# Kernel optimization log

Measured on AMD Instinct MI355X. Metric: run time of the kernel, lower is better.

## Reference

```python
import jax, jax.numpy as jnp
import numpy as np

N_NODES = 100000
N_EDGES = 3200000
NUM_FEATURES = 128
HIDDEN = 16


def _gcn_norm(edge_index, num_nodes):
    # Add self-loops and compute symmetric normalization D^{-1/2} (A+I) D^{-1/2}
    loops = jnp.arange(num_nodes, dtype=edge_index.dtype)
    row = jnp.concatenate([edge_index[0], loops])  # source j
    col = jnp.concatenate([edge_index[1], loops])  # target i
    ones = jnp.ones(row.shape[0], dtype=jnp.float32)
    deg = jax.ops.segment_sum(ones, col, num_segments=num_nodes)
    deg_inv_sqrt = jnp.where(deg > 0, jax.lax.rsqrt(deg), 0.0)
    norm = deg_inv_sqrt[row] * deg_inv_sqrt[col]  # [E + N]
    return row, col, norm


def _gcn_conv(x, row, col, norm, W, b, num_nodes):
    h = x @ W                                   # [N, out] linear first (PyG order)
    msg = h[row] * norm[:, None]                # gather + edge-wise scale
    out = jax.ops.segment_sum(msg, col, num_segments=num_nodes)  # scatter-add
    return out + b                              # bias after aggregation (PyG)


def setup_inputs() -> dict:
    key = jax.random.key(0)
    k1, k2, k3, k4, k5 = jax.random.split(key, 5)
    x = jax.random.normal(k1, (N_NODES, NUM_FEATURES), dtype=jnp.float32)
    edge_index = jax.random.randint(k2, (2, N_EDGES), 0, N_NODES, dtype=jnp.int64)
    # Glorot-style init for GCNConv linear weights
    W1 = jax.random.normal(k3, (NUM_FEATURES, HIDDEN), dtype=jnp.float32) / np.sqrt(NUM_FEATURES)
    b1 = jnp.zeros((HIDDEN,), dtype=jnp.float32)
    W2 = jax.random.normal(k4, (HIDDEN, 1), dtype=jnp.float32) / np.sqrt(HIDDEN)
    b2 = jnp.zeros((1,), dtype=jnp.float32)
    return {"x": x, "edge_index": edge_index, "W1": W1, "b1": b1, "W2": W2, "b2": b2}


def reference(x, edge_index, W1, b1, W2, b2):
    num_nodes = x.shape[0]
    row, col, norm = _gcn_norm(edge_index, num_nodes)  # shared by both layers
    h = _gcn_conv(x, row, col, norm, W1, b1, num_nodes)
    h = jax.nn.relu(h)
    out = _gcn_conv(h, row, col, norm, W2, b2, num_nodes)
    return out
```

## Files before the change

### kernel.cpp

```cpp
#include <hip/hip_runtime.h>
#include <hip/hip_fp16.h>


#define CB 8
#define CAP 9216
#define TILE 4096

__global__ void k_init_gcur(int* __restrict__ gcur, int nb) {
    int b = blockIdx.x * blockDim.x + threadIdx.x;
    if (b < nb) gcur[b] = b * CAP;
}

__global__ void __launch_bounds__(512) k_partition(
        const int* __restrict__ row, const int* __restrict__ col,
        int* __restrict__ gcur, int* __restrict__ ebuf, int e, int nb) {
    __shared__ int hist[512];
    __shared__ int lbase[512];
    __shared__ int gdelta[512];
    __shared__ int sval[TILE];
    __shared__ unsigned short sbkt[TILE];
    const int base = blockIdx.x * TILE;
    const int cnt = min(TILE, e - base);
    const int t = threadIdx.x;
    hist[t] = 0;
    __syncthreads();
#pragma unroll
    for (int k = 0; k < TILE / 512; ++k) {
        int i = base + (k << 9) + t;
        if (i < e) atomicAdd(&hist[col[i] >> CB], 1);
    }
    __syncthreads();
    int v = hist[t];
    lbase[t] = v;
    __syncthreads();
    for (int off = 1; off < 512; off <<= 1) {
        int add = (t >= off) ? lbase[t - off] : 0;
        __syncthreads();
        lbase[t] += add;
        __syncthreads();
    }
    int excl = lbase[t] - v;
    __syncthreads();
    lbase[t] = excl;
    int gb = v ? atomicAdd(&gcur[t], v) : 0;
    gdelta[t] = gb - excl;
    hist[t] = excl;
    __syncthreads();
#pragma unroll
    for (int k = 0; k < TILE / 512; ++k) {
        int i = base + (k << 9) + t;
        if (i < e) {
            int c = col[i], r = row[i];
            int b = c >> CB;
            int p = atomicAdd(&hist[b], 1);
            sval[p] = ((c & ((1 << CB) - 1)) << 17) | r;
            sbkt[p] = (unsigned short)b;
        }
    }
    __syncthreads();
    for (int j = t; j < cnt; j += 512) {
        int b = sbkt[j];
        int p = gdelta[b] + j;
        if (p < (b + 1) * CAP) ebuf[p] = sval[j];
    }
}

__global__ void __launch_bounds__(256) k_bucket(
        const int* __restrict__ ebuf, const int* __restrict__ gcur,
        int* __restrict__ begA, int* __restrict__ endA, int* __restrict__ ssrc,
        float* __restrict__ dis, int n) {
    __shared__ int hist[256];
    __shared__ int sc[256];
    const int b = blockIdx.x, t = threadIdx.x;
    const int base = b * CAP;
    const int cnt = min(gcur[b] - base, CAP);
    hist[t] = 0;
    __syncthreads();
    for (int j = t; j < cnt; j += 256) atomicAdd(&hist[ebuf[base + j] >> 17], 1);
    __syncthreads();
    int v = hist[t];
    sc[t] = v;
    __syncthreads();
    for (int off = 1; off < 256; off <<= 1) {
        int add = (t >= off) ? sc[t - off] : 0;
        __syncthreads();
        sc[t] += add;
        __syncthreads();
    }
    int excl = sc[t] - v;
    int node = (b << CB) + t;
    if (node < n) {
        begA[node] = base + excl;
        endA[node] = base + excl + v;
        dis[node] = rsqrtf((float)(v + 1));
    }
    hist[t] = excl;
    __syncthreads();
    for (int j = t; j < cnt; j += 256) {
        int val = ebuf[base + j];
        int p = atomicAdd(&hist[val >> 17], 1);
        ssrc[base + p] = val & 0x1FFFF;
    }
}

__global__ void k_gemm1(const float* __restrict__ x, const float* __restrict__ W1,
                        const float* __restrict__ dis, __half* __restrict__ gh, int n) {
    __shared__ float wt[16 * 128];
    for (int t = threadIdx.x; t < 2048; t += blockDim.x) {
        int j = t >> 7, k = t & 127;
        wt[t] = W1[k * 16 + j];
    }
    __syncthreads();
    int r = blockIdx.x * blockDim.x + threadIdx.x;
    if (r >= n) return;
    const float4* x4 = (const float4*)(x + (size_t)r * 128);
    const float4* w4 = (const float4*)wt;
    float acc[16];
#pragma unroll
    for (int j = 0; j < 16; ++j) acc[j] = 0.f;
    for (int k4 = 0; k4 < 32; ++k4) {
        float4 vv = x4[k4];
#pragma unroll
        for (int j = 0; j < 16; ++j) {
            float4 w = w4[j * 32 + k4];
            acc[j] += vv.x * w.x + vv.y * w.y + vv.z * w.z + vv.w * w.w;
        }
    }
    float d = dis[r];
    __half2 hh[8];
#pragma unroll
    for (int j = 0; j < 8; ++j)
        hh[j] = __floats2half2_rn(d * acc[2 * j], d * acc[2 * j + 1]);
    uint4* o = (uint4*)(gh + (size_t)r * 16);
    const uint4* src = (const uint4*)hh;
    o[0] = src[0];
    o[1] = src[1];
}

__global__ void k_gather1(const int* __restrict__ begA, const int* __restrict__ endA,
                          const int* __restrict__ ssrc,
                          const __half2* __restrict__ g2, const float* __restrict__ dis,
                          const float* __restrict__ b1, const float* __restrict__ W2,
                          float* __restrict__ tbuf, int n) {
    int t = blockIdx.x * blockDim.x + threadIdx.x;
    if (t >= n * 8) return;
    int i = t >> 3, f2 = t & 7;
    float di = dis[i];
    int beg = begA[i], end = endA[i];
    float2 acc = __half22float2(g2[(size_t)i * 8 + f2]);
    for (int e = beg; e < end; ++e) {
        float2 v = __half22float2(g2[(size_t)ssrc[e] * 8 + f2]);
        acc.x += v.x;
        acc.y += v.y;
    }
    int f = f2 * 2;
    float u = fmaxf(di * acc.x + b1[f], 0.f) * W2[f]
            + fmaxf(di * acc.y + b1[f + 1], 0.f) * W2[f + 1];
#pragma unroll
    for (int m = 4; m >= 1; m >>= 1) u += __shfl_xor(u, m, 8);
    if (f2 == 0) tbuf[i] = di * u;
}

__global__ void k_gather2(const int* __restrict__ begA, const int* __restrict__ endA,
                          const int* __restrict__ ssrc,
                          const float* __restrict__ tbuf, const float* __restrict__ dis,
                          const float* __restrict__ b2, float* __restrict__ out, int n) {
    int t = blockIdx.x * blockDim.x + threadIdx.x;
    if (t >= n * 8) return;
    int i = t >> 3, l = t & 7;
    int beg = begA[i], end = endA[i];
    float acc = (l == 0) ? tbuf[i] : 0.f;
    for (int e = beg + l; e < end; e += 8) acc += tbuf[ssrc[e]];
#pragma unroll
    for (int m = 4; m >= 1; m >>= 1) acc += __shfl_xor(acc, m, 8);
    if (l == 0) out[i] = dis[i] * acc + b2[0];
}

extern "C" void kernel_launch(void* const* d_in, const int* in_sizes, int n_in,
                              void* d_out, int out_size, void* d_ws, size_t ws_size,
                              hipStream_t stream) {
    const float* x  = (const float*)d_in[0];
    const int*   ei = (const int*)d_in[1];
    const float* W1 = (const float*)d_in[2];
    const float* b1 = (const float*)d_in[3];
    const float* W2 = (const float*)d_in[4];
    const float* b2 = (const float*)d_in[5];
    float* out = (float*)d_out;

    const int N = in_sizes[0] / 128;
    const int E = in_sizes[1] / 2;
    const int* row = ei;
    const int* col = ei + E;
    const int NB = (N + 255) >> CB;
    const size_t PADE = (size_t)NB * CAP;

    size_t bigsz = PADE > (size_t)N * 8 ? PADE : (size_t)N * 8;
    int*    ebuf = (int*)d_ws;
    __half* gh   = (__half*)d_ws;
    int*    ssrc = (int*)d_ws + bigsz;
    float*  dis  = (float*)(ssrc + PADE);
    float*  tbuf = dis + N;
    int*    begA = (int*)(tbuf + N);
    int*    endA = begA + N;
    int*    gcur = endA + N;

    auto cdiv = [](int a, int b) { return (a + b - 1) / b; };

    k_init_gcur<<<cdiv(NB, 256),    256, 0, stream>>>(gcur, NB);
    k_partition<<<cdiv(E, TILE),    512, 0, stream>>>(row, col, gcur, ebuf, E, NB);
    k_bucket   <<<NB,               256, 0, stream>>>(ebuf, gcur, begA, endA, ssrc, dis, N);
    k_gemm1    <<<cdiv(N, 256),     256, 0, stream>>>(x, W1, dis, gh, N);
    k_gather1  <<<cdiv(N * 8, 256), 256, 0, stream>>>(begA, endA, ssrc, (const __half2*)gh,
                                                      dis, b1, W2, tbuf, N);
    k_gather2  <<<cdiv(N * 8, 256), 256, 0, stream>>>(begA, endA, ssrc, tbuf, dis, b2, out, N);
}
```

Baseline: 238.9 us.

## Replace per-node CSR build with bucket-level LDS atomic aggregation

Drops the second counting-sort pass inside each 256-node bucket, along with the begA/endA/ssrc arrays. The k_bucket kernel shrinks to a degree-only kernel. Both aggregation layers now run one 1024-thread block per bucket: each block streams the bucket's unsorted edges, gathers the source features with one-step prefetch, and accumulates into shared memory with float atomics before applying the epilogue. This removes the per-node segment walk and the scatter of sorted indices. In exchange it relies on heavy LDS float atomics, 16 per edge in layer 1, which may contend, and it makes the summation order nondeterministic.

```diff
diff --git a/kernel.cpp b/kernel.cpp
--- a/kernel.cpp
+++ b/kernel.cpp
@@ -65,12 +65,10 @@
     }
 }
 
-__global__ void __launch_bounds__(256) k_bucket(
+__global__ void __launch_bounds__(256) k_deg(
         const int* __restrict__ ebuf, const int* __restrict__ gcur,
-        int* __restrict__ begA, int* __restrict__ endA, int* __restrict__ ssrc,
         float* __restrict__ dis, int n) {
     __shared__ int hist[256];
-    __shared__ int sc[256];
     const int b = blockIdx.x, t = threadIdx.x;
     const int base = b * CAP;
     const int cnt = min(gcur[b] - base, CAP);
@@ -78,29 +76,8 @@
     __syncthreads();
     for (int j = t; j < cnt; j += 256) atomicAdd(&hist[ebuf[base + j] >> 17], 1);
     __syncthreads();
-    int v = hist[t];
-    sc[t] = v;
-    __syncthreads();
-    for (int off = 1; off < 256; off <<= 1) {
-        int add = (t >= off) ? sc[t - off] : 0;
-        __syncthreads();
-        sc[t] += add;
-        __syncthreads();
-    }
-    int excl = sc[t] - v;
     int node = (b << CB) + t;
-    if (node < n) {
-        begA[node] = base + excl;
-        endA[node] = base + excl + v;
-        dis[node] = rsqrtf((float)(v + 1));
-    }
-    hist[t] = excl;
-    __syncthreads();
-    for (int j = t; j < cnt; j += 256) {
-        int val = ebuf[base + j];
-        int p = atomicAdd(&hist[val >> 17], 1);
-        ssrc[base + p] = val & 0x1FFFF;
-    }
+    if (node < n) dis[node] = rsqrtf((float)(hist[t] + 1));
 }
 
 __global__ void k_gemm1(const float* __restrict__ x, const float* __restrict__ W1,
@@ -137,43 +114,102 @@
     o[1] = src[1];
 }
 
-__global__ void k_gather1(const int* __restrict__ begA, const int* __restrict__ endA,
-                          const int* __restrict__ ssrc,
-                          const __half2* __restrict__ g2, const float* __restrict__ dis,
-                          const float* __restrict__ b1, const float* __restrict__ W2,
-                          float* __restrict__ tbuf, int n) {
-    int t = blockIdx.x * blockDim.x + threadIdx.x;
-    if (t >= n * 8) return;
-    int i = t >> 3, f2 = t & 7;
-    float di = dis[i];
-    int beg = begA[i], end = endA[i];
-    float2 acc = __half22float2(g2[(size_t)i * 8 + f2]);
-    for (int e = beg; e < end; ++e) {
-        float2 v = __half22float2(g2[(size_t)ssrc[e] * 8 + f2]);
-        acc.x += v.x;
-        acc.y += v.y;
-    }
-    int f = f2 * 2;
-    float u = fmaxf(di * acc.x + b1[f], 0.f) * W2[f]
-            + fmaxf(di * acc.y + b1[f + 1], 0.f) * W2[f + 1];
-#pragma unroll
-    for (int m = 4; m >= 1; m >>= 1) u += __shfl_xor(u, m, 8);
-    if (f2 == 0) tbuf[i] = di * u;
-}
-
-__global__ void k_gather2(const int* __restrict__ begA, const int* __restrict__ endA,
-                          const int* __restrict__ ssrc,
-                          const float* __restrict__ tbuf, const float* __restrict__ dis,
-                          const float* __restrict__ b2, float* __restrict__ out, int n) {
-    int t = blockIdx.x * blockDim.x + threadIdx.x;
-    if (t >= n * 8) return;
-    int i = t >> 3, l = t & 7;
-    int beg = begA[i], end = endA[i];
-    float acc = (l == 0) ? tbuf[i] : 0.f;
-    for (int e = beg + l; e < end; e += 8) acc += tbuf[ssrc[e]];
-#pragma unroll
-    for (int m = 4; m >= 1; m >>= 1) acc += __shfl_xor(acc, m, 8);
-    if (l == 0) out[i] = dis[i] * acc + b2[0];
+__device__ inline void unpack8(uint4 u, float* f) {
+    const __half2* h = (const __half2*)&u;
+#pragma unroll
+    for (int k = 0; k < 4; ++k) {
+        float2 t2 = __half22float2(h[k]);
+        f[2 * k] = t2.x;
+        f[2 * k + 1] = t2.y;
+    }
+}
+
+__global__ void __launch_bounds__(1024) k_fused1(
+        const int* __restrict__ ebuf, const int* __restrict__ gcur,
+        const uint4* __restrict__ gq, const float* __restrict__ dis,
+        const float* __restrict__ b1, const float* __restrict__ W2,
+        float* __restrict__ tbuf, int n) {
+    __shared__ float agg[256 * 17];
+    __shared__ float sB[16], sW[16];
+    const int b = blockIdx.x, t = threadIdx.x;
+    const int base = b * CAP;
+    const int cnt = min(gcur[b] - base, CAP);
+    for (int j = t; j < 256 * 17; j += 1024) agg[j] = 0.f;
+    if (t < 16) { sB[t] = b1[t]; sW[t] = W2[t]; }
+    __syncthreads();
+    int j = t, v = 0;
+    uint4 u0, u1;
+    if (j < cnt) {
+        v = ebuf[base + j];
+        int s = v & 0x1FFFF;
+        u0 = gq[(size_t)s * 2];
+        u1 = gq[(size_t)s * 2 + 1];
+    }
+    while (j < cnt) {
+        int jn = j + 1024, vn = 0;
+        uint4 n0, n1;
+        if (jn < cnt) {
+            vn = ebuf[base + jn];
+            int s = vn & 0x1FFFF;
+            n0 = gq[(size_t)s * 2];
+            n1 = gq[(size_t)s * 2 + 1];
+        }
+        float f[16];
+        unpack8(u0, f);
+        unpack8(u1, f + 8);
+        float* a = &agg[(v >> 17) * 17];
+#pragma unroll
+        for (int k = 0; k < 16; ++k) atomicAdd(&a[k], f[k]);
+        j = jn; v = vn; u0 = n0; u1 = n1;
+    }
+    __syncthreads();
+    if (t < 256) {
+        int node = (b << CB) + t;
+        if (node < n) {
+            float di = dis[node];
+            float self[16];
+            unpack8(gq[(size_t)node * 2], self);
+            unpack8(gq[(size_t)node * 2 + 1], self + 8);
+            float u = 0.f;
+#pragma unroll
+            for (int f = 0; f < 16; ++f)
+                u += fmaxf(di * (agg[t * 17 + f] + self[f]) + sB[f], 0.f) * sW[f];
+            tbuf[node] = di * u;
+        }
+    }
+}
+
+__global__ void __launch_bounds__(1024) k_fused2(
+        const int* __restrict__ ebuf, const int* __restrict__ gcur,
+        const float* __restrict__ tbuf, const float* __restrict__ dis,
+        const float* __restrict__ b2, float* __restrict__ out, int n) {
+    __shared__ float sagg[256];
+    const int b = blockIdx.x, t = threadIdx.x;
+    const int base = b * CAP;
+    const int cnt = min(gcur[b] - base, CAP);
+    if (t < 256) sagg[t] = 0.f;
+    __syncthreads();
+    int j = t, v = 0;
+    float tv = 0.f;
+    if (j < cnt) {
+        v = ebuf[base + j];
+        tv = tbuf[v & 0x1FFFF];
+    }
+    while (j < cnt) {
+        int jn = j + 1024, vn = 0;
+        float tn = 0.f;
+        if (jn < cnt) {
+            vn = ebuf[base + jn];
+            tn = tbuf[vn & 0x1FFFF];
+        }
+        atomicAdd(&sagg[v >> 17], tv);
+        j = jn; v = vn; tv = tn;
+    }
+    __syncthreads();
+    if (t < 256) {
+        int node = (b << CB) + t;
+        if (node < n) out[node] = dis[node] * (sagg[t] + tbuf[node]) + b2[0];
+    }
 }
 
 extern "C" void kernel_launch(void* const* d_in, const int* in_sizes, int n_in,
@@ -194,23 +230,19 @@
     const int NB = (N + 255) >> CB;
     const size_t PADE = (size_t)NB * CAP;
 
-    size_t bigsz = PADE > (size_t)N * 8 ? PADE : (size_t)N * 8;
     int*    ebuf = (int*)d_ws;
-    __half* gh   = (__half*)d_ws;
-    int*    ssrc = (int*)d_ws + bigsz;
-    float*  dis  = (float*)(ssrc + PADE);
+    __half* gh   = (__half*)((int*)d_ws + PADE);
+    float*  dis  = (float*)((int*)d_ws + PADE + (size_t)N * 8);
     float*  tbuf = dis + N;
-    int*    begA = (int*)(tbuf + N);
-    int*    endA = begA + N;
-    int*    gcur = endA + N;
+    int*    gcur = (int*)(tbuf + N);
 
     auto cdiv = [](int a, int b) { return (a + b - 1) / b; };
 
-    k_init_gcur<<<cdiv(NB, 256),    256, 0, stream>>>(gcur, NB);
-    k_partition<<<cdiv(E, TILE),    512, 0, stream>>>(row, col, gcur, ebuf, E, NB);
-    k_bucket   <<<NB,               256, 0, stream>>>(ebuf, gcur, begA, endA, ssrc, dis, N);
-    k_gemm1    <<<cdiv(N, 256),     256, 0, stream>>>(x, W1, dis, gh, N);
-    k_gather1  <<<cdiv(N * 8, 256), 256, 0, stream>>>(begA, endA, ssrc, (const __half2*)gh,
-                                                      dis, b1, W2, tbuf, N);
-    k_gather2  <<<cdiv(N * 8, 256), 256, 0, stream>>>(begA, endA, ssrc, tbuf, dis, b2, out, N);
-}
+    k_init_gcur<<<cdiv(NB, 256), 256,  0, stream>>>(gcur, NB);
+    k_partition<<<cdiv(E, TILE), 512,  0, stream>>>(row, col, gcur, ebuf, E, NB);
+    k_deg      <<<NB,            256,  0, stream>>>(ebuf, gcur, dis, N);
+    k_gemm1    <<<cdiv(N, 256),  256,  0, stream>>>(x, W1, dis, gh, N);
+    k_fused1   <<<NB,            1024, 0, stream>>>(ebuf, gcur, (const uint4*)gh,
+                                                    dis, b1, W2, tbuf, N);
+    k_fused2   <<<NB,            1024, 0, stream>>>(ebuf, gcur, tbuf, dis, b2, out, N);
+}
```

New measurement: 524.0 us. 2.19x slower.
